# Kernel optimization log

Measured on AMD Instinct MI355X. Metric: run time of the kernel, lower is better.

## Reference

```python
import jax, jax.numpy as jnp
import numpy as np

B = 8
N_GENES = 19836
D_IN = 11
D_H = 64
DEG = 16
N = B * N_GENES
E_PER = N_GENES * DEG


def setup_inputs() -> dict:
    key = jax.random.key(0)
    ks = jax.random.split(key, 20)
    x = jax.random.normal(ks[0], (B, N_GENES, D_IN), dtype=jnp.float32)
    # edges: random within each graph, offset by graph index
    base_src = jax.random.randint(ks[1], (B, E_PER), 0, N_GENES)
    base_dst = jax.random.randint(ks[2], (B, E_PER), 0, N_GENES)
    offs = (jnp.arange(B) * N_GENES)[:, None]
    src = (base_src + offs).reshape(-1).astype(jnp.int64) if False else (base_src + offs).reshape(-1)
    dst = (base_dst + offs).reshape(-1)
    s = 0.02
    def nrm(k, shape):
        return jax.random.normal(k, shape, dtype=jnp.float32) * s
    return {
        'x': x, 'src': src, 'dst': dst,
        'enc_W': nrm(ks[3], (D_H, D_IN)), 'enc_b': jnp.zeros((D_H,), jnp.float32),
        'gene_emb': nrm(ks[4], (N_GENES, D_H)),
        'gin_W': nrm(ks[5], (D_H, D_H)),
        'bn_w': 1.0 + nrm(ks[6], (D_H,)), 'bn_b': jnp.zeros((D_H,), jnp.float32),
        'key_W': nrm(ks[7], (D_H, D_H)), 'key_b': jnp.zeros((D_H,), jnp.float32),
        'query_w': nrm(ks[8], (1, D_H)),
        'val_W': nrm(ks[9], (D_H, D_H)), 'val_b': jnp.zeros((D_H,), jnp.float32),
        'sae_enc_W': nrm(ks[10], (D_H, D_H)), 'sae_enc_b': jnp.zeros((D_H,), jnp.float32),
        'sae_dec_W': nrm(ks[11], (D_H, D_H)), 'sae_dec_b': jnp.zeros((D_H,), jnp.float32),
        'pred_W1': nrm(ks[12], (D_H, D_H)), 'pred_b1': jnp.zeros((D_H,), jnp.float32),
        'pred_W2': nrm(ks[13], (1, D_H)), 'pred_b2': jnp.zeros((1,), jnp.float32),
    }


def gelu(x):
    return jax.nn.gelu(x, approximate=False)  # nn.GELU default = exact erf


def batchnorm(h, w, b, eps=1e-5):
    # training-mode BatchNorm1d: batch statistics, biased variance
    mu = jnp.mean(h, axis=0)
    var = jnp.mean((h - mu) ** 2, axis=0)
    return (h - mu) * jax.lax.rsqrt(var + eps) * w + b


def reference(x, src, dst, enc_W, enc_b, gene_emb, gin_W, bn_w, bn_b,
              key_W, key_b, query_w, val_W, val_b,
              sae_enc_W, sae_enc_b, sae_dec_W, sae_dec_b,
              pred_W1, pred_b1, pred_W2, pred_b2):
    bsz, n_gene, d_in = x.shape
    n_nodes = bsz * n_gene
    # gene encoder: single Linear (bias) + GELU (inner batchnorm result is discarded in source)
    h = gelu(x.reshape(-1, d_in) @ enc_W.T + enc_b)          # [N, D_H]
    h = (h.reshape(bsz, n_gene, -1) + gene_emb).reshape(n_nodes, -1)
    # GIN layer (eps=0, sum aggregation): MLP(h + sum_{u->v} h_u); MLP = single Linear, no bias
    agg = jax.ops.segment_sum(h[src], dst, num_segments=n_nodes)  # irregular gather/scatter
    h = (h + agg) @ gin_W.T
    h = gelu(batchnorm(h, bn_w, bn_b))
    # attentive readout with SAE
    keys = h @ key_W.T + key_b
    w = jax.nn.sigmoid(keys @ query_w.T)                     # [N, 1]
    v = h @ val_W.T + val_b
    z = v * w
    enc = jax.nn.relu(z @ sae_enc_W.T + sae_enc_b)
    dec = enc @ sae_dec_W.T + sae_dec_b
    sae_loss = jnp.mean((dec - z) ** 2) + 1.0 * jnp.mean(jnp.abs(enc))
    gid = jnp.arange(n_nodes) // n_gene
    g_h = jax.ops.segment_sum(dec * w, gid, num_segments=bsz)  # [B, D_H]
    # predictor: Linear+GELU, Linear (inner batchnorm discarded in source)
    preds = gelu(g_h @ pred_W1.T + pred_b1) @ pred_W2.T + pred_b2
    return preds, w, sae_loss, dec
```

## Files before the change

kernel.cpp:

```cpp
#include <hip/hip_runtime.h>
#include <math.h>

#define NGENES 19836
#define BATCH 8
#define DIN 11
#define DH 64
#define NNODES (BATCH * NGENES)
#define NEDGES (NNODES * 16)
#define NDH (NNODES * DH)

#define SCAN_CHUNK 1024
#define NSBLK ((NNODES + SCAN_CHUNK - 1) / SCAN_CHUNK)

#define OUT_PREDS 0
#define OUT_W 8
#define OUT_SAE (8 + NNODES)
#define OUT_DEC (9 + NNODES)

__device__ __forceinline__ float gelu_f(float x) {
    return 0.5f * x * (1.0f + erff(x * 0.70710678118654752f));
}

__device__ __forceinline__ float bcast(float v, int lane) {
    return __int_as_float(__builtin_amdgcn_readlane(__float_as_int(v), lane));
}

__device__ __forceinline__ float wave_sum(float v) {
    #pragma unroll
    for (int o = 32; o; o >>= 1) v += __shfl_xor(v, o, 64);
    return v;
}

__global__ void k_encoder(const float* __restrict__ x, const float* __restrict__ encW,
                          const float* __restrict__ encB, const float* __restrict__ gemb,
                          float* __restrict__ h) {
    int lane = threadIdx.x & 63;
    int wid = (blockIdx.x * blockDim.x + threadIdx.x) >> 6;
    int tw = (gridDim.x * blockDim.x) >> 6;
    int chunk = (NNODES + tw - 1) / tw;
    int start = wid * chunk;
    int end = min(start + chunk, NNODES);
    float wreg[DIN];
    #pragma unroll
    for (int k = 0; k < DIN; ++k) wreg[k] = encW[lane * DIN + k];
    float bias = encB[lane];
    for (int node = start; node < end; ++node) {
        const float* xr = x + (size_t)node * DIN;
        float acc = bias;
        #pragma unroll
        for (int k = 0; k < DIN; ++k) acc = fmaf(xr[k], wreg[k], acc);
        int gene = node % NGENES;
        h[(size_t)node * DH + lane] = gelu_f(acc) + gemb[(size_t)gene * DH + lane];
    }
}

__global__ void k_hist(const int* __restrict__ dst, int* __restrict__ counts) {
    int i = blockIdx.x * blockDim.x + threadIdx.x;
    int stride = gridDim.x * blockDim.x;
    for (int e = i; e < NEDGES; e += stride)
        atomicAdd(&counts[dst[e]], 1);
}

__global__ void k_scan1(const int* __restrict__ counts, int* __restrict__ bsum) {
    __shared__ int red[256];
    int base = blockIdx.x * SCAN_CHUNK + threadIdx.x * 4;
    int s = 0;
    #pragma unroll
    for (int i = 0; i < 4; ++i) {
        int n = base + i;
        if (n < NNODES) s += counts[n];
    }
    red[threadIdx.x] = s;
    __syncthreads();
    for (int o = 128; o; o >>= 1) {
        if (threadIdx.x < o) red[threadIdx.x] += red[threadIdx.x + o];
        __syncthreads();
    }
    if (threadIdx.x == 0) bsum[blockIdx.x] = red[0];
}

__global__ void k_scan2(const int* __restrict__ bsum, int* __restrict__ boff) {
    if (threadIdx.x == 0) {
        int acc = 0;
        for (int i = 0; i < NSBLK; ++i) { boff[i] = acc; acc += bsum[i]; }
    }
}

__global__ void k_scan3(const int* __restrict__ counts, const int* __restrict__ boff,
                        int* __restrict__ offsets, int* __restrict__ cursor) {
    __shared__ int red[256];
    int t = threadIdx.x;
    int base = blockIdx.x * SCAN_CHUNK + t * 4;
    int c[4];
    int s = 0;
    #pragma unroll
    for (int i = 0; i < 4; ++i) {
        int n = base + i;
        c[i] = (n < NNODES) ? counts[n] : 0;
        s += c[i];
    }
    red[t] = s;
    __syncthreads();
    for (int o = 1; o < 256; o <<= 1) {
        int v = (t >= o) ? red[t - o] : 0;
        __syncthreads();
        red[t] += v;
        __syncthreads();
    }
    int excl = red[t] - s + boff[blockIdx.x];
    #pragma unroll
    for (int i = 0; i < 4; ++i) {
        int n = base + i;
        if (n < NNODES) { offsets[n] = excl; cursor[n] = excl; }
        excl += c[i];
    }
}

__global__ void k_scatter(const int* __restrict__ src, const int* __restrict__ dst,
                          int* __restrict__ cursor, unsigned short* __restrict__ csr) {
    int i = blockIdx.x * blockDim.x + threadIdx.x;
    int stride = gridDim.x * blockDim.x;
    for (int e = i; e < NEDGES; e += stride) {
        int p = atomicAdd(&cursor[dst[e]], 1);
        csr[p] = (unsigned short)(src[e] % NGENES);
    }
}

__global__ void k_aggin(const float* __restrict__ h, const int* __restrict__ offsets,
                        const int* __restrict__ counts, const unsigned short* __restrict__ csr,
                        const float* __restrict__ ginW, float* __restrict__ h2,
                        float* __restrict__ stats) {
    int lane = threadIdx.x & 63;
    int wid = (blockIdx.x * blockDim.x + threadIdx.x) >> 6;
    int tw = (gridDim.x * blockDim.x) >> 6;
    float wr[DH];
    #pragma unroll
    for (int k = 0; k < DH; ++k) wr[k] = ginW[lane * DH + k];
    float s1 = 0.f, s2 = 0.f;
    for (int node = wid; node < NNODES; node += tw) {
        int gbase = (node / NGENES) * NGENES;
        float a0 = h[(size_t)node * DH + lane], a1 = 0.f, a2 = 0.f, a3 = 0.f;
        int start = offsets[node];
        int cnt = counts[node];
        for (int e0 = 0; e0 < cnt; e0 += 64) {
            int nn = min(64, cnt - e0);
            int iv = (lane < nn) ? (int)csr[start + e0 + lane] : 0;
            int j = 0;
            for (; j + 3 < nn; j += 4) {
                int v0 = gbase + __shfl(iv, j, 64);
                int v1 = gbase + __shfl(iv, j + 1, 64);
                int v2 = gbase + __shfl(iv, j + 2, 64);
                int v3 = gbase + __shfl(iv, j + 3, 64);
                a0 += h[(size_t)v0 * DH + lane];
                a1 += h[(size_t)v1 * DH + lane];
                a2 += h[(size_t)v2 * DH + lane];
                a3 += h[(size_t)v3 * DH + lane];
            }
            for (; j < nn; ++j)
                a0 += h[(size_t)(gbase + __shfl(iv, j, 64)) * DH + lane];
        }
        float tval = (a0 + a1) + (a2 + a3);
        float m0 = 0.f, m1 = 0.f;
        #pragma unroll
        for (int k = 0; k < DH; k += 2) {
            m0 = fmaf(wr[k], bcast(tval, k), m0);
            m1 = fmaf(wr[k + 1], bcast(tval, k + 1), m1);
        }
        float outv = m0 + m1;
        h2[(size_t)node * DH + lane] = outv;
        s1 += outv;
        s2 += outv * outv;
    }
    __shared__ float red[2][256];
    red[0][threadIdx.x] = s1;
    red[1][threadIdx.x] = s2;
    __syncthreads();
    if (threadIdx.x < 64) {
        float t1 = red[0][threadIdx.x] + red[0][threadIdx.x + 64] + red[0][threadIdx.x + 128] + red[0][threadIdx.x + 192];
        float t2 = red[1][threadIdx.x] + red[1][threadIdx.x + 64] + red[1][threadIdx.x + 128] + red[1][threadIdx.x + 192];
        atomicAdd(&stats[threadIdx.x], t1);
        atomicAdd(&stats[64 + threadIdx.x], t2);
    }
}

__global__ void k_bnparams(const float* __restrict__ stats, const float* __restrict__ bnw,
                           const float* __restrict__ bnb, float* __restrict__ bnp) {
    int d = threadIdx.x;
    float inv_n = 1.0f / (float)NNODES;
    float mu = stats[d] * inv_n;
    float var = stats[64 + d] * inv_n - mu * mu;
    float sc = bnw[d] * rsqrtf(var + 1e-5f);
    bnp[d] = sc;
    bnp[64 + d] = bnb[d] - mu * sc;
}

__global__ void k_attn(float* __restrict__ h2, const float* __restrict__ bnp,
                       const float* __restrict__ keyW, const float* __restrict__ keyB,
                       const float* __restrict__ qw, const float* __restrict__ valW,
                       const float* __restrict__ valB, float* __restrict__ wout) {
    int lane = threadIdx.x & 63;
    int wid = (blockIdx.x * blockDim.x + threadIdx.x) >> 6;
    int tw = (gridDim.x * blockDim.x) >> 6;
    int chunk = (NNODES + tw - 1) / tw;
    int start = wid * chunk;
    int end = min(start + chunk, NNODES);
    float kw[DH], vw[DH];
    #pragma unroll
    for (int k = 0; k < DH; ++k) {
        kw[k] = keyW[lane * DH + k];
        vw[k] = valW[lane * DH + k];
    }
    float kb = keyB[lane], vb = valB[lane], qv = qw[lane];
    float sc = bnp[lane], sh = bnp[64 + lane];
    for (int node = start; node < end; ++node) {
        float hv = h2[(size_t)node * DH + lane];
        float h3 = gelu_f(fmaf(hv, sc, sh));
        float ka0 = 0.f, ka1 = 0.f, va0 = 0.f, va1 = 0.f;
        #pragma unroll
        for (int k = 0; k < DH; k += 2) {
            float b0 = bcast(h3, k);
            float b1 = bcast(h3, k + 1);
            ka0 = fmaf(kw[k], b0, ka0);
            va0 = fmaf(vw[k], b0, va0);
            ka1 = fmaf(kw[k + 1], b1, ka1);
            va1 = fmaf(vw[k + 1], b1, va1);
        }
        float keys = ka0 + ka1 + kb;
        float p = wave_sum(keys * qv);
        float wq = 1.0f / (1.0f + expf(-p));
        float z = (va0 + va1 + vb) * wq;
        h2[(size_t)node * DH + lane] = z;
        if (lane == 0) wout[node] = wq;
    }
}

__global__ void k_sae(const float* __restrict__ zbuf, const float* __restrict__ encW,
                      const float* __restrict__ encB, const float* __restrict__ decW,
                      const float* __restrict__ decB, const float* __restrict__ wout,
                      float* __restrict__ decout, float* __restrict__ g_h,
                      float* __restrict__ loss) {
    int lane = threadIdx.x & 63;
    int wid = (blockIdx.x * blockDim.x + threadIdx.x) >> 6;
    int tw = (gridDim.x * blockDim.x) >> 6;
    int chunk = (NNODES + tw - 1) / tw;
    int start = wid * chunk;
    int end = min(start + chunk, NNODES);
    float ew[DH], dw[DH];
    #pragma unroll
    for (int k = 0; k < DH; ++k) {
        ew[k] = encW[lane * DH + k];
        dw[k] = decW[lane * DH + k];
    }
    float eb = encB[lane], db = decB[lane];
    float sq = 0.f, l1 = 0.f, gacc = 0.f;
    int cur_g = (start < NNODES) ? (start / NGENES) : 0;
    for (int node = start; node < end; ++node) {
        float z = zbuf[(size_t)node * DH + lane];
        float ea0 = 0.f, ea1 = 0.f;
        #pragma unroll
        for (int k = 0; k < DH; k += 2) {
            ea0 = fmaf(ew[k], bcast(z, k), ea0);
            ea1 = fmaf(ew[k + 1], bcast(z, k + 1), ea1);
        }
        float enc = fmaxf(ea0 + ea1 + eb, 0.0f);
        float da0 = 0.f, da1 = 0.f;
        #pragma unroll
        for (int k = 0; k < DH; k += 2) {
            da0 = fmaf(dw[k], bcast(enc, k), da0);
            da1 = fmaf(dw[k + 1], bcast(enc, k + 1), da1);
        }
        float dec = da0 + da1 + db;
        float wq = wout[node];
        decout[(size_t)node * DH + lane] = dec;
        float diff = dec - z;
        sq = fmaf(diff, diff, sq);
        l1 += fabsf(enc);
        int g = node / NGENES;
        if (g != cur_g) {
            atomicAdd(&g_h[cur_g * DH + lane], gacc);
            gacc = 0.f;
            cur_g = g;
        }
        gacc = fmaf(dec, wq, gacc);
    }
    if (start < end) atomicAdd(&g_h[cur_g * DH + lane], gacc);
    sq = wave_sum(sq);
    l1 = wave_sum(l1);
    if (lane == 0) {
        atomicAdd(&loss[0], sq);
        atomicAdd(&loss[1], l1);
    }
}

__global__ void k_pred(const float* __restrict__ g_h, const float* __restrict__ W1,
                       const float* __restrict__ b1, const float* __restrict__ W2,
                       const float* __restrict__ b2, const float* __restrict__ loss,
                       float* __restrict__ out) {
    int lane = threadIdx.x;
    float w1[DH];
    #pragma unroll
    for (int k = 0; k < DH; ++k) w1[k] = W1[lane * DH + k];
    float bb = b1[lane], w2 = W2[lane];
    for (int g = 0; g < BATCH; ++g) {
        float gh = g_h[g * DH + lane];
        float a0 = 0.f, a1 = 0.f;
        #pragma unroll
        for (int k = 0; k < DH; k += 2) {
            a0 = fmaf(w1[k], bcast(gh, k), a0);
            a1 = fmaf(w1[k + 1], bcast(gh, k + 1), a1);
        }
        float t = gelu_f(a0 + a1 + bb);
        float p = wave_sum(t * w2);
        if (lane == 0) out[OUT_PREDS + g] = p + b2[0];
    }
    if (lane == 0) out[OUT_SAE] = (loss[0] + loss[1]) * (1.0f / ((float)NNODES * (float)DH));
}

extern "C" void kernel_launch(void* const* d_in, const int* in_sizes, int n_in,
                              void* d_out, int out_size, void* d_ws, size_t ws_size,
                              hipStream_t stream) {
    const float* x    = (const float*)d_in[0];
    const int* src    = (const int*)d_in[1];
    const int* dst    = (const int*)d_in[2];
    const float* encW = (const float*)d_in[3];
    const float* encB = (const float*)d_in[4];
    const float* gemb = (const float*)d_in[5];
    const float* ginW = (const float*)d_in[6];
    const float* bnw  = (const float*)d_in[7];
    const float* bnb  = (const float*)d_in[8];
    const float* keyW = (const float*)d_in[9];
    const float* keyB = (const float*)d_in[10];
    const float* qw   = (const float*)d_in[11];
    const float* valW = (const float*)d_in[12];
    const float* valB = (const float*)d_in[13];
    const float* saeEncW = (const float*)d_in[14];
    const float* saeEncB = (const float*)d_in[15];
    const float* saeDecW = (const float*)d_in[16];
    const float* saeDecB = (const float*)d_in[17];
    const float* pW1  = (const float*)d_in[18];
    const float* pb1  = (const float*)d_in[19];
    const float* pW2  = (const float*)d_in[20];
    const float* pb2  = (const float*)d_in[21];

    float* out = (float*)d_out;
    float* ws = (float*)d_ws;

    int*   counts  = (int*)ws;
    float* stats   = ws + NNODES;
    float* g_h     = stats + 128;
    float* loss    = g_h + 512;
    float* bnp     = loss + 2;
    int*   offsets = (int*)(bnp + 128);
    int*   cursor  = offsets + NNODES;
    unsigned short* csr = (unsigned short*)(cursor + NNODES);
    int*   bsum    = (int*)(csr + NEDGES);
    int*   boff    = bsum + 256;
    float* h2      = (float*)(boff + 256);

    float* h    = out + OUT_DEC;
    float* wout = out + OUT_W;

    hipMemsetAsync(d_ws, 0, (size_t)(NNODES + 770) * sizeof(float), stream);

    k_encoder<<<2048, 256, 0, stream>>>(x, encW, encB, gemb, h);
    k_hist<<<4096, 256, 0, stream>>>(dst, counts);
    k_scan1<<<NSBLK, 256, 0, stream>>>(counts, bsum);
    k_scan2<<<1, 64, 0, stream>>>(bsum, boff);
    k_scan3<<<NSBLK, 256, 0, stream>>>(counts, boff, offsets, cursor);
    k_scatter<<<4096, 256, 0, stream>>>(src, dst, cursor, csr);
    k_aggin<<<2048, 256, 0, stream>>>(h, offsets, counts, csr, ginW, h2, stats);
    k_bnparams<<<1, 64, 0, stream>>>(stats, bnw, bnb, bnp);
    k_attn<<<1024, 256, 0, stream>>>(h2, bnp, keyW, keyB, qw, valW, valB, wout);
    k_sae<<<1024, 256, 0, stream>>>(h2, saeEncW, saeEncB, saeDecW, saeDecB, wout, h, g_h, loss);
    k_pred<<<1, 64, 0, stream>>>(g_h, pW1, pb1, pW2, pb2, loss, out);
}
```

Before: 985.4 us.

## Fold key projection into query vector, batch 4 nodes per wave, parallelize block scan

Precomputes keyW^T·q and q·keyB once in the BN-params kernel, so the attention kernel replaces the per-node 64x64 key matvec with a dot product. The attention and SAE kernels now process four nodes per iteration, reusing each register-held weight across four broadcasts and issuing independent reductions. The serial single-thread block-offset scan becomes a 256-thread parallel scan. The aggregation loop unrolls to 8 independent gather accumulators, and several grid sizes change. Register pressure rises and the summation order differs slightly.

```diff
diff --git a/kernel.cpp b/kernel.cpp
--- a/kernel.cpp
+++ b/kernel.cpp
@@ -8,6 +8,7 @@
 #define NNODES (BATCH * NGENES)
 #define NEDGES (NNODES * 16)
 #define NDH (NNODES * DH)
+#define NGRP (NNODES / 4)
 
 #define SCAN_CHUNK 1024
 #define NSBLK ((NNODES + SCAN_CHUNK - 1) / SCAN_CHUNK)
@@ -80,10 +81,18 @@
 }
 
 __global__ void k_scan2(const int* __restrict__ bsum, int* __restrict__ boff) {
-    if (threadIdx.x == 0) {
-        int acc = 0;
-        for (int i = 0; i < NSBLK; ++i) { boff[i] = acc; acc += bsum[i]; }
-    }
+    __shared__ int red[256];
+    int t = threadIdx.x;
+    int v = (t < NSBLK) ? bsum[t] : 0;
+    red[t] = v;
+    __syncthreads();
+    for (int o = 1; o < 256; o <<= 1) {
+        int u = (t >= o) ? red[t - o] : 0;
+        __syncthreads();
+        red[t] += u;
+        __syncthreads();
+    }
+    if (t < NSBLK) boff[t] = red[t] - v;
 }
 
 __global__ void k_scan3(const int* __restrict__ counts, const int* __restrict__ boff,
@@ -139,34 +148,36 @@
     float s1 = 0.f, s2 = 0.f;
     for (int node = wid; node < NNODES; node += tw) {
         int gbase = (node / NGENES) * NGENES;
-        float a0 = h[(size_t)node * DH + lane], a1 = 0.f, a2 = 0.f, a3 = 0.f;
+        float a[8];
+        a[0] = h[(size_t)node * DH + lane];
+        #pragma unroll
+        for (int i = 1; i < 8; ++i) a[i] = 0.f;
         int start = offsets[node];
         int cnt = counts[node];
         for (int e0 = 0; e0 < cnt; e0 += 64) {
             int nn = min(64, cnt - e0);
             int iv = (lane < nn) ? (int)csr[start + e0 + lane] : 0;
             int j = 0;
-            for (; j + 3 < nn; j += 4) {
-                int v0 = gbase + __shfl(iv, j, 64);
-                int v1 = gbase + __shfl(iv, j + 1, 64);
-                int v2 = gbase + __shfl(iv, j + 2, 64);
-                int v3 = gbase + __shfl(iv, j + 3, 64);
-                a0 += h[(size_t)v0 * DH + lane];
-                a1 += h[(size_t)v1 * DH + lane];
-                a2 += h[(size_t)v2 * DH + lane];
-                a3 += h[(size_t)v3 * DH + lane];
+            for (; j + 7 < nn; j += 8) {
+                #pragma unroll
+                for (int u = 0; u < 8; ++u) {
+                    int v = gbase + __shfl(iv, j + u, 64);
+                    a[u] += h[(size_t)v * DH + lane];
+                }
             }
             for (; j < nn; ++j)
-                a0 += h[(size_t)(gbase + __shfl(iv, j, 64)) * DH + lane];
-        }
-        float tval = (a0 + a1) + (a2 + a3);
-        float m0 = 0.f, m1 = 0.f;
-        #pragma unroll
-        for (int k = 0; k < DH; k += 2) {
+                a[0] += h[(size_t)(gbase + __shfl(iv, j, 64)) * DH + lane];
+        }
+        float tval = ((a[0] + a[1]) + (a[2] + a[3])) + ((a[4] + a[5]) + (a[6] + a[7]));
+        float m0 = 0.f, m1 = 0.f, m2 = 0.f, m3 = 0.f;
+        #pragma unroll
+        for (int k = 0; k < DH; k += 4) {
             m0 = fmaf(wr[k], bcast(tval, k), m0);
             m1 = fmaf(wr[k + 1], bcast(tval, k + 1), m1);
-        }
-        float outv = m0 + m1;
+            m2 = fmaf(wr[k + 2], bcast(tval, k + 2), m2);
+            m3 = fmaf(wr[k + 3], bcast(tval, k + 3), m3);
+        }
+        float outv = (m0 + m1) + (m2 + m3);
         h2[(size_t)node * DH + lane] = outv;
         s1 += outv;
         s2 += outv * outv;
@@ -184,7 +195,9 @@
 }
 
 __global__ void k_bnparams(const float* __restrict__ stats, const float* __restrict__ bnw,
-                           const float* __restrict__ bnb, float* __restrict__ bnp) {
+                           const float* __restrict__ bnb, const float* __restrict__ keyW,
+                           const float* __restrict__ keyB, const float* __restrict__ qw,
+                           float* __restrict__ bnp) {
     int d = threadIdx.x;
     float inv_n = 1.0f / (float)NNODES;
     float mu = stats[d] * inv_n;
@@ -192,45 +205,63 @@
     float sc = bnw[d] * rsqrtf(var + 1e-5f);
     bnp[d] = sc;
     bnp[64 + d] = bnb[d] - mu * sc;
+    float kq0 = 0.f, kq1 = 0.f;
+    #pragma unroll
+    for (int j = 0; j < DH; j += 2) {
+        kq0 = fmaf(qw[j], keyW[j * DH + d], kq0);
+        kq1 = fmaf(qw[j + 1], keyW[(j + 1) * DH + d], kq1);
+    }
+    bnp[128 + d] = kq0 + kq1;
+    float qb = wave_sum(qw[d] * keyB[d]);
+    if (d == 0) bnp[192] = qb;
 }
 
 __global__ void k_attn(float* __restrict__ h2, const float* __restrict__ bnp,
-                       const float* __restrict__ keyW, const float* __restrict__ keyB,
-                       const float* __restrict__ qw, const float* __restrict__ valW,
-                       const float* __restrict__ valB, float* __restrict__ wout) {
+                       const float* __restrict__ valW, const float* __restrict__ valB,
+                       float* __restrict__ wout) {
     int lane = threadIdx.x & 63;
     int wid = (blockIdx.x * blockDim.x + threadIdx.x) >> 6;
     int tw = (gridDim.x * blockDim.x) >> 6;
-    int chunk = (NNODES + tw - 1) / tw;
-    int start = wid * chunk;
-    int end = min(start + chunk, NNODES);
-    float kw[DH], vw[DH];
-    #pragma unroll
-    for (int k = 0; k < DH; ++k) {
-        kw[k] = keyW[lane * DH + k];
-        vw[k] = valW[lane * DH + k];
-    }
-    float kb = keyB[lane], vb = valB[lane], qv = qw[lane];
-    float sc = bnp[lane], sh = bnp[64 + lane];
-    for (int node = start; node < end; ++node) {
-        float hv = h2[(size_t)node * DH + lane];
-        float h3 = gelu_f(fmaf(hv, sc, sh));
-        float ka0 = 0.f, ka1 = 0.f, va0 = 0.f, va1 = 0.f;
-        #pragma unroll
-        for (int k = 0; k < DH; k += 2) {
-            float b0 = bcast(h3, k);
-            float b1 = bcast(h3, k + 1);
-            ka0 = fmaf(kw[k], b0, ka0);
-            va0 = fmaf(vw[k], b0, va0);
-            ka1 = fmaf(kw[k + 1], b1, ka1);
-            va1 = fmaf(vw[k + 1], b1, va1);
-        }
-        float keys = ka0 + ka1 + kb;
-        float p = wave_sum(keys * qv);
-        float wq = 1.0f / (1.0f + expf(-p));
-        float z = (va0 + va1 + vb) * wq;
-        h2[(size_t)node * DH + lane] = z;
-        if (lane == 0) wout[node] = wq;
+    int chunk = (NGRP + tw - 1) / tw;
+    int gs = wid * chunk;
+    int ge = min(gs + chunk, NGRP);
+    float vw[DH];
+    #pragma unroll
+    for (int k = 0; k < DH; ++k) vw[k] = valW[lane * DH + k];
+    float vb = valB[lane], sc = bnp[lane], sh = bnp[64 + lane], kq = bnp[128 + lane];
+    float qb = bnp[192];
+    for (int g = gs; g < ge; ++g) {
+        int node = g * 4;
+        float h3[4], p[4];
+        #pragma unroll
+        for (int i = 0; i < 4; ++i) {
+            float hv = h2[(size_t)(node + i) * DH + lane];
+            h3[i] = gelu_f(fmaf(hv, sc, sh));
+            p[i] = h3[i] * kq;
+        }
+        #pragma unroll
+        for (int o = 32; o; o >>= 1) {
+            #pragma unroll
+            for (int i = 0; i < 4; ++i) p[i] += __shfl_xor(p[i], o, 64);
+        }
+        float wq[4];
+        #pragma unroll
+        for (int i = 0; i < 4; ++i) wq[i] = 1.0f / (1.0f + expf(-(p[i] + qb)));
+        float a[4];
+        #pragma unroll
+        for (int i = 0; i < 4; ++i) a[i] = 0.f;
+        #pragma unroll
+        for (int k = 0; k < DH; ++k) {
+            #pragma unroll
+            for (int i = 0; i < 4; ++i) a[i] = fmaf(vw[k], bcast(h3[i], k), a[i]);
+        }
+        #pragma unroll
+        for (int i = 0; i < 4; ++i)
+            h2[(size_t)(node + i) * DH + lane] = (a[i] + vb) * wq[i];
+        if (lane == 0) {
+            wout[node] = wq[0]; wout[node + 1] = wq[1];
+            wout[node + 2] = wq[2]; wout[node + 3] = wq[3];
+        }
     }
 }
 
@@ -242,9 +273,9 @@
     int lane = threadIdx.x & 63;
     int wid = (blockIdx.x * blockDim.x + threadIdx.x) >> 6;
     int tw = (gridDim.x * blockDim.x) >> 6;
-    int chunk = (NNODES + tw - 1) / tw;
-    int start = wid * chunk;
-    int end = min(start + chunk, NNODES);
+    int chunk = (NGRP + tw - 1) / tw;
+    int gs = wid * chunk;
+    int ge = min(gs + chunk, NGRP);
     float ew[DH], dw[DH];
     #pragma unroll
     for (int k = 0; k < DH; ++k) {
@@ -253,37 +284,48 @@
     }
     float eb = encB[lane], db = decB[lane];
     float sq = 0.f, l1 = 0.f, gacc = 0.f;
-    int cur_g = (start < NNODES) ? (start / NGENES) : 0;
-    for (int node = start; node < end; ++node) {
-        float z = zbuf[(size_t)node * DH + lane];
-        float ea0 = 0.f, ea1 = 0.f;
-        #pragma unroll
-        for (int k = 0; k < DH; k += 2) {
-            ea0 = fmaf(ew[k], bcast(z, k), ea0);
-            ea1 = fmaf(ew[k + 1], bcast(z, k + 1), ea1);
-        }
-        float enc = fmaxf(ea0 + ea1 + eb, 0.0f);
-        float da0 = 0.f, da1 = 0.f;
-        #pragma unroll
-        for (int k = 0; k < DH; k += 2) {
-            da0 = fmaf(dw[k], bcast(enc, k), da0);
-            da1 = fmaf(dw[k + 1], bcast(enc, k + 1), da1);
-        }
-        float dec = da0 + da1 + db;
-        float wq = wout[node];
-        decout[(size_t)node * DH + lane] = dec;
-        float diff = dec - z;
-        sq = fmaf(diff, diff, sq);
-        l1 += fabsf(enc);
-        int g = node / NGENES;
-        if (g != cur_g) {
+    int cur_g = (gs < NGRP) ? (gs * 4) / NGENES : 0;
+    for (int g = gs; g < ge; ++g) {
+        int node = g * 4;
+        int gg = node / NGENES;
+        if (gg != cur_g) {
             atomicAdd(&g_h[cur_g * DH + lane], gacc);
             gacc = 0.f;
-            cur_g = g;
-        }
-        gacc = fmaf(dec, wq, gacc);
-    }
-    if (start < end) atomicAdd(&g_h[cur_g * DH + lane], gacc);
+            cur_g = gg;
+        }
+        float z[4], e[4], enc[4], d[4];
+        #pragma unroll
+        for (int i = 0; i < 4; ++i) {
+            z[i] = zbuf[(size_t)(node + i) * DH + lane];
+            e[i] = 0.f;
+        }
+        #pragma unroll
+        for (int k = 0; k < DH; ++k) {
+            #pragma unroll
+            for (int i = 0; i < 4; ++i) e[i] = fmaf(ew[k], bcast(z[i], k), e[i]);
+        }
+        #pragma unroll
+        for (int i = 0; i < 4; ++i) {
+            enc[i] = fmaxf(e[i] + eb, 0.0f);
+            d[i] = 0.f;
+        }
+        #pragma unroll
+        for (int k = 0; k < DH; ++k) {
+            #pragma unroll
+            for (int i = 0; i < 4; ++i) d[i] = fmaf(dw[k], bcast(enc[i], k), d[i]);
+        }
+        #pragma unroll
+        for (int i = 0; i < 4; ++i) {
+            float dec = d[i] + db;
+            float wq = wout[node + i];
+            decout[(size_t)(node + i) * DH + lane] = dec;
+            float diff = dec - z[i];
+            sq = fmaf(diff, diff, sq);
+            l1 += fabsf(enc[i]);
+            gacc = fmaf(dec, wq, gacc);
+        }
+    }
+    if (gs < ge) atomicAdd(&g_h[cur_g * DH + lane], gacc);
     sq = wave_sum(sq);
     l1 = wave_sum(l1);
     if (lane == 0) {
@@ -350,7 +392,7 @@
     float* g_h     = stats + 128;
     float* loss    = g_h + 512;
     float* bnp     = loss + 2;
-    int*   offsets = (int*)(bnp + 128);
+    int*   offsets = (int*)(bnp + 256);
     int*   cursor  = offsets + NNODES;
     unsigned short* csr = (unsigned short*)(cursor + NNODES);
     int*   bsum    = (int*)(csr + NEDGES);
@@ -360,17 +402,17 @@
     float* h    = out + OUT_DEC;
     float* wout = out + OUT_W;
 
-    hipMemsetAsync(d_ws, 0, (size_t)(NNODES + 770) * sizeof(float), stream);
+    hipMemsetAsync(d_ws, 0, (size_t)(NNODES + 642) * sizeof(float), stream);
 
     k_encoder<<<2048, 256, 0, stream>>>(x, encW, encB, gemb, h);
-    k_hist<<<4096, 256, 0, stream>>>(dst, counts);
+    k_hist<<<2048, 256, 0, stream>>>(dst, counts);
     k_scan1<<<NSBLK, 256, 0, stream>>>(counts, bsum);
-    k_scan2<<<1, 64, 0, stream>>>(bsum, boff);
+    k_scan2<<<1, 256, 0, stream>>>(bsum, boff);
     k_scan3<<<NSBLK, 256, 0, stream>>>(counts, boff, offsets, cursor);
-    k_scatter<<<4096, 256, 0, stream>>>(src, dst, cursor, csr);
+    k_scatter<<<2048, 256, 0, stream>>>(src, dst, cursor, csr);
     k_aggin<<<2048, 256, 0, stream>>>(h, offsets, counts, csr, ginW, h2, stats);
-    k_bnparams<<<1, 64, 0, stream>>>(stats, bnw, bnb, bnp);
-    k_attn<<<1024, 256, 0, stream>>>(h2, bnp, keyW, keyB, qw, valW, valB, wout);
-    k_sae<<<1024, 256, 0, stream>>>(h2, saeEncW, saeEncB, saeDecW, saeDecB, wout, h, g_h, loss);
+    k_bnparams<<<1, 64, 0, stream>>>(stats, bnw, bnb, keyW, keyB, qw, bnp);
+    k_attn<<<2048, 256, 0, stream>>>(h2, bnp, valW, valB, wout);
+    k_sae<<<2048, 256, 0, stream>>>(h2, saeEncW, saeEncB, saeDecW, saeDecB, wout, h, g_h, loss);
     k_pred<<<1, 64, 0, stream>>>(g_h, pW1, pb1, pW2, pb2, loss, out);
 }
```

New measurement: 1.191 ms. +20.9%, slower.
